# Kernel tuning notes

Measured on AMD Instinct MI355X. Metric: run time of the kernel, lower is better.

## Reference

```python
import jax, jax.numpy as jnp
import numpy as np

WINDOW = 3
SEQ_LEN = 41
FEATURE = 128
FILTER_NUM = 128
PAD = WINDOW // 2


def setup_inputs() -> dict:
    key = jax.random.key(0)
    k1, k2 = jax.random.split(key)
    B = 4096
    inputs = jax.random.normal(k1, (B, SEQ_LEN, FEATURE), dtype=jnp.float32)
    # per-position Linear weights: 41 independent [window*feature -> filter_num] layers
    fan_in = WINDOW * FEATURE
    W = jax.random.normal(k2, (SEQ_LEN, fan_in, FILTER_NUM), dtype=jnp.float32) / np.sqrt(fan_in)
    b = jnp.zeros((SEQ_LEN, FILTER_NUM), dtype=jnp.float32)
    return {"inputs": inputs, "W": W, "b": b}


def reference(inputs, W, b):
    # inputs: [B, S, F]; pad sequence dim by PAD zeros on each side
    xpad = jnp.pad(inputs, ((0, 0), (PAD, PAD), (0, 0)))  # [B, S+2*PAD, F]
    # gather windows: idx[s, w] = s + w -> [B, S, WINDOW, F]
    idx = jnp.arange(SEQ_LEN)[:, None] + jnp.arange(WINDOW)[None, :]
    xw = xpad[:, idx, :]
    B = inputs.shape[0]
    xw = xw.reshape(B, SEQ_LEN, WINDOW * FEATURE)  # [B, S, W*F]
    # per-position linear (locally-connected): one batched GEMM over positions
    out = jnp.einsum('bsd,sdf->bsf', xw, W) + b[None, :, :]
    # ReLU; Dropout(0.5) is identity in eval mode
    return jax.nn.relu(out)
```

## Files before the change

kernel.cpp:

```cpp
#include <hip/hip_runtime.h>
#include <hip/hip_bf16.h>

#define SEQ 41
#define FEAT 128
#define KDIM 384
#define BM 64
#define BK 64
#define LDA (BK + 8)
#define LDB (BK + 8)

typedef float floatx4 __attribute__((ext_vector_type(4)));
typedef __bf16 bf16x8 __attribute__((ext_vector_type(8)));
typedef unsigned short ushortx8 __attribute__((ext_vector_type(8)));

__device__ __forceinline__ unsigned short f2bf(float f) {
    unsigned int u = __builtin_bit_cast(unsigned int, f);
    unsigned int r = (u + 0x7fffu + ((u >> 16) & 1u)) >> 16;
    return (unsigned short)r;
}

__global__ __launch_bounds__(256) void wt_kernel(const float* __restrict__ W,
                                                 unsigned short* __restrict__ Wt) {
    int t = blockIdx.x * 256 + threadIdx.x;
    int n  = t & (FEAT - 1);
    int r  = t >> 7;
    int k0 = (r % (KDIM / 8)) * 8;
    int s  = r / (KDIM / 8);
    const float* Ws = W + (size_t)s * KDIM * FEAT;
    ushortx8 v;
#pragma unroll
    for (int j = 0; j < 8; j++) v[j] = f2bf(Ws[(size_t)(k0 + j) * FEAT + n]);
    *reinterpret_cast<ushortx8*>(Wt + ((size_t)(s * FEAT + n)) * KDIM + k0) = v;
}

template <int USE_WT>
__global__ __launch_bounds__(256) void gemm_kernel(const float* __restrict__ X,
                                                   const void* __restrict__ Wsrc,
                                                   const float* __restrict__ bias,
                                                   float* __restrict__ out) {
    __shared__ unsigned short Alds[BM][LDA];
    __shared__ unsigned short Blds[FEAT][LDB];

    const int tid = threadIdx.x;
    const int s   = blockIdx.y;
    const int m0  = blockIdx.x * BM;

    const int lane = tid & 63;
    const int wv   = tid >> 6;
    const int colq = lane & 15;
    const int quad = lane >> 4;
    const int arow = 16 * wv + colq;

    floatx4 acc[8];
#pragma unroll
    for (int nt = 0; nt < 8; nt++) acc[nt] = (floatx4){0.f, 0.f, 0.f, 0.f};

    const int a_row = tid & 63;
    const int a_seg = tid >> 6;
    const float* xrow = X + (size_t)(m0 + a_row) * (SEQ * FEAT);

    for (int kk = 0; kk < KDIM; kk += BK) {
        {
            int kbase = kk + a_seg * 16;
            int toff  = (s - 1) * FEAT + kbase;
            ushortx8 lo, hi;
#pragma unroll
            for (int j = 0; j < 4; j++) {
                int o = toff + j * 4;
                floatx4 v = (floatx4){0.f, 0.f, 0.f, 0.f};
                if (o >= 0 && o < SEQ * FEAT)
                    v = *reinterpret_cast<const floatx4*>(xrow + o);
#pragma unroll
                for (int e = 0; e < 4; e++) {
                    unsigned short b = f2bf(v[e]);
                    if (j < 2) lo[j * 4 + e] = b; else hi[(j - 2) * 4 + e] = b;
                }
            }
            *reinterpret_cast<ushortx8*>(&Alds[a_row][a_seg * 16])     = lo;
            *reinterpret_cast<ushortx8*>(&Alds[a_row][a_seg * 16 + 8]) = hi;
        }
        if (USE_WT) {
            const unsigned short* Wt = (const unsigned short*)Wsrc;
#pragma unroll
            for (int i = 0; i < 4; i++) {
                int chunk = i * 256 + tid;
                int n  = chunk >> 3;
                int c8 = (chunk & 7) << 3;
                ushortx8 v = *reinterpret_cast<const ushortx8*>(
                    Wt + ((size_t)(s * FEAT + n)) * KDIM + kk + c8);
                *reinterpret_cast<ushortx8*>(&Blds[n][c8]) = v;
            }
        } else {
            const float* Wf = (const float*)Wsrc;
#pragma unroll
            for (int i = 0; i < 8; i++) {
                int q  = i * 256 + tid;
                int n4 = (q & 31) * 4;
                int c  = q >> 5;
                floatx4 v = *reinterpret_cast<const floatx4*>(
                    Wf + ((size_t)(s * KDIM) + kk + c) * FEAT + n4);
#pragma unroll
                for (int j = 0; j < 4; j++) Blds[n4 + j][c] = f2bf(v[j]);
            }
        }
        __syncthreads();

#pragma unroll
        for (int ks = 0; ks < 2; ks++) {
            bf16x8 av = *reinterpret_cast<const bf16x8*>(&Alds[arow][ks * 32 + quad * 8]);
#pragma unroll
            for (int nt = 0; nt < 8; nt++) {
                bf16x8 bv = *reinterpret_cast<const bf16x8*>(
                    &Blds[nt * 16 + colq][ks * 32 + quad * 8]);
                acc[nt] = __builtin_amdgcn_mfma_f32_16x16x32_bf16(av, bv, acc[nt], 0, 0, 0);
            }
        }
        __syncthreads();
    }

    const int m_base = m0 + 16 * wv + quad * 4;
#pragma unroll
    for (int nt = 0; nt < 8; nt++) {
        int n = nt * 16 + colq;
        float bv = bias[s * FEAT + n];
#pragma unroll
        for (int r = 0; r < 4; r++) {
            float v = acc[nt][r] + bv;
            v = v > 0.f ? v : 0.f;
            out[((size_t)(m_base + r) * SEQ + s) * FEAT + n] = v;
        }
    }
}

extern "C" void kernel_launch(void* const* d_in, const int* in_sizes, int n_in,
                              void* d_out, int out_size, void* d_ws, size_t ws_size,
                              hipStream_t stream) {
    const float* X    = (const float*)d_in[0];
    const float* W    = (const float*)d_in[1];
    const float* bias = (const float*)d_in[2];
    float* out = (float*)d_out;

    const int B = in_sizes[0] / (SEQ * FEAT);
    dim3 grid(B / BM, SEQ);

    const size_t wt_bytes = (size_t)SEQ * FEAT * KDIM * sizeof(unsigned short);
    if (ws_size >= wt_bytes) {
        unsigned short* Wt = (unsigned short*)d_ws;
        wt_kernel<<<(SEQ * FEAT * (KDIM / 8) + 255) / 256, 256, 0, stream>>>(W, Wt);
        gemm_kernel<1><<<grid, 256, 0, stream>>>(X, (const void*)Wt, bias, out);
    } else {
        gemm_kernel<0><<<grid, 256, 0, stream>>>(X, (const void*)W, bias, out);
    }
}
```

Baseline: 210.2 us.

## Replace LDS-tiled GEMM with register-direct 32x32 MFMA and software prefetch

Drops shared-memory staging and barriers. Each wave now loads its A and B fragments directly from global memory into registers and feeds 32x32x16 bf16 MFMAs, with a one-step register prefetch of the next k-slice. The grid is reordered so the position index varies fastest, letting blocks that share input rows run close together, and each block covers 128 rows. In exchange, each wave reads B straight from global or L2 with no reuse through LDS, and the A loads are narrower per-lane accesses.

After: 256.9 us. +22.2%, slower.

```diff
diff --git a/kernel.cpp b/kernel.cpp
--- a/kernel.cpp
+++ b/kernel.cpp
@@ -4,12 +4,11 @@
 #define SEQ 41
 #define FEAT 128
 #define KDIM 384
-#define BM 64
-#define BK 64
-#define LDA (BK + 8)
-#define LDB (BK + 8)
+#define ROWLEN (SEQ * FEAT)
+#define KSTEPS (KDIM / 16)
 
 typedef float floatx4 __attribute__((ext_vector_type(4)));
+typedef float floatx16 __attribute__((ext_vector_type(16)));
 typedef __bf16 bf16x8 __attribute__((ext_vector_type(8)));
 typedef unsigned short ushortx8 __attribute__((ext_vector_type(8)));
 
@@ -17,6 +16,13 @@
     unsigned int u = __builtin_bit_cast(unsigned int, f);
     unsigned int r = (u + 0x7fffu + ((u >> 16) & 1u)) >> 16;
     return (unsigned short)r;
+}
+
+__device__ __forceinline__ bf16x8 cvt8(floatx4 lo, floatx4 hi) {
+    ushortx8 u;
+#pragma unroll
+    for (int j = 0; j < 4; j++) { u[j] = f2bf(lo[j]); u[4 + j] = f2bf(hi[j]); }
+    return __builtin_bit_cast(bf16x8, u);
 }
 
 __global__ __launch_bounds__(256) void wt_kernel(const float* __restrict__ W,
@@ -38,98 +44,88 @@
                                                    const void* __restrict__ Wsrc,
                                                    const float* __restrict__ bias,
                                                    float* __restrict__ out) {
-    __shared__ unsigned short Alds[BM][LDA];
-    __shared__ unsigned short Blds[FEAT][LDB];
-
-    const int tid = threadIdx.x;
-    const int s   = blockIdx.y;
-    const int m0  = blockIdx.x * BM;
-
+    const int tid  = threadIdx.x;
     const int lane = tid & 63;
     const int wv   = tid >> 6;
-    const int colq = lane & 15;
-    const int quad = lane >> 4;
-    const int arow = 16 * wv + colq;
+    const int s    = blockIdx.x;
+    const int mblk = blockIdx.y;
+    const int nl   = lane & 31;
+    const int kh   = lane >> 5;
 
-    floatx4 acc[8];
+    const int row = mblk * 128 + wv * 32 + nl;
+    const float* xrow = X + (size_t)row * ROWLEN;
+    const int obase = (s - 1) * FEAT + kh * 8;
+
+    const unsigned short* Wt = (const unsigned short*)Wsrc;
+    const float* Wf = (const float*)Wsrc;
+
+    floatx16 acc[4];
 #pragma unroll
-    for (int nt = 0; nt < 8; nt++) acc[nt] = (floatx4){0.f, 0.f, 0.f, 0.f};
+    for (int nt = 0; nt < 4; nt++) acc[nt] = (floatx16)(0.f);
 
-    const int a_row = tid & 63;
-    const int a_seg = tid >> 6;
-    const float* xrow = X + (size_t)(m0 + a_row) * (SEQ * FEAT);
+    floatx4 a_lo, a_hi;
+    ushortx8 bq[4];
 
-    for (int kk = 0; kk < KDIM; kk += BK) {
-        {
-            int kbase = kk + a_seg * 16;
-            int toff  = (s - 1) * FEAT + kbase;
-            ushortx8 lo, hi;
-#pragma unroll
-            for (int j = 0; j < 4; j++) {
-                int o = toff + j * 4;
-                floatx4 v = (floatx4){0.f, 0.f, 0.f, 0.f};
-                if (o >= 0 && o < SEQ * FEAT)
-                    v = *reinterpret_cast<const floatx4*>(xrow + o);
-#pragma unroll
-                for (int e = 0; e < 4; e++) {
-                    unsigned short b = f2bf(v[e]);
-                    if (j < 2) lo[j * 4 + e] = b; else hi[(j - 2) * 4 + e] = b;
-                }
-            }
-            *reinterpret_cast<ushortx8*>(&Alds[a_row][a_seg * 16])     = lo;
-            *reinterpret_cast<ushortx8*>(&Alds[a_row][a_seg * 16 + 8]) = hi;
-        }
-        if (USE_WT) {
-            const unsigned short* Wt = (const unsigned short*)Wsrc;
-#pragma unroll
-            for (int i = 0; i < 4; i++) {
-                int chunk = i * 256 + tid;
-                int n  = chunk >> 3;
-                int c8 = (chunk & 7) << 3;
-                ushortx8 v = *reinterpret_cast<const ushortx8*>(
-                    Wt + ((size_t)(s * FEAT + n)) * KDIM + kk + c8);
-                *reinterpret_cast<ushortx8*>(&Blds[n][c8]) = v;
-            }
-        } else {
-            const float* Wf = (const float*)Wsrc;
-#pragma unroll
-            for (int i = 0; i < 8; i++) {
-                int q  = i * 256 + tid;
-                int n4 = (q & 31) * 4;
-                int c  = q >> 5;
-                floatx4 v = *reinterpret_cast<const floatx4*>(
-                    Wf + ((size_t)(s * KDIM) + kk + c) * FEAT + n4);
-#pragma unroll
-                for (int j = 0; j < 4; j++) Blds[n4 + j][c] = f2bf(v[j]);
-            }
-        }
-        __syncthreads();
-
-#pragma unroll
-        for (int ks = 0; ks < 2; ks++) {
-            bf16x8 av = *reinterpret_cast<const bf16x8*>(&Alds[arow][ks * 32 + quad * 8]);
-#pragma unroll
-            for (int nt = 0; nt < 8; nt++) {
-                bf16x8 bv = *reinterpret_cast<const bf16x8*>(
-                    &Blds[nt * 16 + colq][ks * 32 + quad * 8]);
-                acc[nt] = __builtin_amdgcn_mfma_f32_16x16x32_bf16(av, bv, acc[nt], 0, 0, 0);
-            }
-        }
-        __syncthreads();
+#define LOAD_A(ks)                                                        \
+    {                                                                     \
+        int o = obase + (ks) * 16;                                        \
+        a_lo = (floatx4)(0.f); a_hi = (floatx4)(0.f);                     \
+        if (o >= 0 && o < ROWLEN) {                                       \
+            a_lo = *reinterpret_cast<const floatx4*>(xrow + o);           \
+            a_hi = *reinterpret_cast<const floatx4*>(xrow + o + 4);       \
+        }                                                                 \
+    }
+#define LOAD_B(ks)                                                              \
+    if (USE_WT) {                                                               \
+        _Pragma("unroll")                                                       \
+        for (int nt = 0; nt < 4; nt++)                                          \
+            bq[nt] = *reinterpret_cast<const ushortx8*>(                        \
+                Wt + ((size_t)(s * FEAT + nt * 32 + nl)) * KDIM + (ks) * 16 + kh * 8); \
+    } else {                                                                    \
+        _Pragma("unroll")                                                       \
+        for (int nt = 0; nt < 4; nt++) {                                        \
+            _Pragma("unroll")                                                   \
+            for (int j = 0; j < 8; j++)                                         \
+                bq[nt][j] = f2bf(Wf[((size_t)s * KDIM + (ks) * 16 + kh * 8 + j) * FEAT \
+                                    + nt * 32 + nl]);                           \
+        }                                                                       \
     }
 
-    const int m_base = m0 + 16 * wv + quad * 4;
+    LOAD_A(0);
+    LOAD_B(0);
+
+#pragma unroll 4
+    for (int ks = 0; ks < KSTEPS; ks++) {
+        bf16x8 av = cvt8(a_lo, a_hi);
+        bf16x8 bv0 = __builtin_bit_cast(bf16x8, bq[0]);
+        bf16x8 bv1 = __builtin_bit_cast(bf16x8, bq[1]);
+        bf16x8 bv2 = __builtin_bit_cast(bf16x8, bq[2]);
+        bf16x8 bv3 = __builtin_bit_cast(bf16x8, bq[3]);
+        if (ks + 1 < KSTEPS) {
+            LOAD_A(ks + 1);
+            LOAD_B(ks + 1);
+        }
+        acc[0] = __builtin_amdgcn_mfma_f32_32x32x16_bf16(av, bv0, acc[0], 0, 0, 0);
+        acc[1] = __builtin_amdgcn_mfma_f32_32x32x16_bf16(av, bv1, acc[1], 0, 0, 0);
+        acc[2] = __builtin_amdgcn_mfma_f32_32x32x16_bf16(av, bv2, acc[2], 0, 0, 0);
+        acc[3] = __builtin_amdgcn_mfma_f32_32x32x16_bf16(av, bv3, acc[3], 0, 0, 0);
+    }
+
+    const int mbase = mblk * 128 + wv * 32 + 4 * kh;
 #pragma unroll
-    for (int nt = 0; nt < 8; nt++) {
-        int n = nt * 16 + colq;
+    for (int nt = 0; nt < 4; nt++) {
+        int n = nt * 32 + nl;
         float bv = bias[s * FEAT + n];
 #pragma unroll
-        for (int r = 0; r < 4; r++) {
+        for (int r = 0; r < 16; r++) {
+            int m = mbase + (r & 3) + 8 * (r >> 2);
             float v = acc[nt][r] + bv;
             v = v > 0.f ? v : 0.f;
-            out[((size_t)(m_base + r) * SEQ + s) * FEAT + n] = v;
+            out[((size_t)m * SEQ + s) * FEAT + n] = v;
         }
     }
+#undef LOAD_A
+#undef LOAD_B
 }
 
 extern "C" void kernel_launch(void* const* d_in, const int* in_sizes, int n_in,
@@ -140,8 +136,8 @@
     const float* bias = (const float*)d_in[2];
     float* out = (float*)d_out;
 
-    const int B = in_sizes[0] / (SEQ * FEAT);
-    dim3 grid(B / BM, SEQ);
+    const int B = in_sizes[0] / ROWLEN;
+    dim3 grid(SEQ, B / 128);
 
     const size_t wt_bytes = (size_t)SEQ * FEAT * KDIM * sizeof(unsigned short);
     if (ws_size >= wt_bytes) {
```

## Double-buffer GEMM with fragment-ordered LDS, direct-to-LDS weight loads, and edge K-skip

Applied to the files above, without the earlier changes.

Rewrites the locally-connected GEMM to use a 128-row tile with a 2x2 wave layout, each wave computing a 4x4 grid of MFMA tiles. Weights are pre-permuted into MFMA fragment order so they can be copied global-to-LDS with direct DMA loads, and A tiles are written in fragment order. A register/LDS double buffer overlaps the next slab's loads with the current MFMAs, and K slabs that are entirely zero padding are skipped at the first and last sequence positions. The trade-off is more registers and LDS per block (launch bounds set to 2 blocks per CU) and halved grid size.

Result: faster. 184.2 us (-12.4%).

```diff
diff --git a/kernel.cpp b/kernel.cpp
--- a/kernel.cpp
+++ b/kernel.cpp
@@ -1,133 +1,170 @@
 #include <hip/hip_runtime.h>
-#include <hip/hip_bf16.h>
 
 #define SEQ 41
 #define FEAT 128
 #define KDIM 384
-#define BM 64
-#define BK 64
-#define LDA (BK + 8)
-#define LDB (BK + 8)
+#define ROWLEN (SEQ * FEAT)
+#define BM 128
 
 typedef float floatx4 __attribute__((ext_vector_type(4)));
 typedef __bf16 bf16x8 __attribute__((ext_vector_type(8)));
+typedef unsigned short ushortx4 __attribute__((ext_vector_type(4)));
 typedef unsigned short ushortx8 __attribute__((ext_vector_type(8)));
 
 __device__ __forceinline__ unsigned short f2bf(float f) {
     unsigned int u = __builtin_bit_cast(unsigned int, f);
-    unsigned int r = (u + 0x7fffu + ((u >> 16) & 1u)) >> 16;
-    return (unsigned short)r;
+    return (unsigned short)((u + 0x7fffu + ((u >> 16) & 1u)) >> 16);
 }
 
-__global__ __launch_bounds__(256) void wt_kernel(const float* __restrict__ W,
-                                                 unsigned short* __restrict__ Wt) {
+#define DMA16(g, l)                                                          \
+    __builtin_amdgcn_global_load_lds(                                        \
+        (const __attribute__((address_space(1))) void*)(g),                  \
+        (__attribute__((address_space(3))) void*)(l), 16, 0, 0)
+
+__global__ __launch_bounds__(256) void wt2_kernel(const float* __restrict__ W,
+                                                  unsigned short* __restrict__ Wt2) {
     int t = blockIdx.x * 256 + threadIdx.x;
-    int n  = t & (FEAT - 1);
-    int r  = t >> 7;
-    int k0 = (r % (KDIM / 8)) * 8;
-    int s  = r / (KDIM / 8);
+    int s = t / 6144, g = t % 6144;
+    int lane = g & 63, nt = (g >> 6) & 7, ks = (g >> 9) & 1, slab = g >> 10;
+    int n  = nt * 16 + (lane & 15);
+    int k0 = slab * 64 + ks * 32 + (lane >> 4) * 8;
     const float* Ws = W + (size_t)s * KDIM * FEAT;
     ushortx8 v;
 #pragma unroll
     for (int j = 0; j < 8; j++) v[j] = f2bf(Ws[(size_t)(k0 + j) * FEAT + n]);
-    *reinterpret_cast<ushortx8*>(Wt + ((size_t)(s * FEAT + n)) * KDIM + k0) = v;
+    *reinterpret_cast<ushortx8*>(Wt2 + (size_t)t * 8) = v;
 }
 
 template <int USE_WT>
-__global__ __launch_bounds__(256) void gemm_kernel(const float* __restrict__ X,
-                                                   const void* __restrict__ Wsrc,
-                                                   const float* __restrict__ bias,
-                                                   float* __restrict__ out) {
-    __shared__ unsigned short Alds[BM][LDA];
-    __shared__ unsigned short Blds[FEAT][LDB];
+__global__ __launch_bounds__(256, 2) void gemm_kernel(const float* __restrict__ X,
+                                                      const void* __restrict__ Wsrc,
+                                                      const float* __restrict__ bias,
+                                                      float* __restrict__ out) {
+    __shared__ unsigned short Afrag[2][2][8][512];
+    __shared__ unsigned short Bfrag[2][2][8][512];
 
-    const int tid = threadIdx.x;
-    const int s   = blockIdx.y;
-    const int m0  = blockIdx.x * BM;
-
+    const int tid  = threadIdx.x;
     const int lane = tid & 63;
     const int wv   = tid >> 6;
-    const int colq = lane & 15;
-    const int quad = lane >> 4;
-    const int arow = 16 * wv + colq;
+    const int s    = blockIdx.y;
+    const int m0   = blockIdx.x * BM;
 
-    floatx4 acc[8];
+    const int klo = (s == 0) ? 2 : 0;
+    const int khi = (s == SEQ - 1) ? 4 : 6;
+    const int nk  = khi - klo;
+    const int obase = (s - 1) * FEAT;
+
+    const int colq = lane & 15, quad = lane >> 4;
+    const int wr = wv >> 1, wc = wv & 1;
+
+    const int ar = tid >> 3;
+    const int ag = tid & 7;
+    const int aq = ag >> 1, ahalf = ag & 1;
+
+    const unsigned short* Wt2 = (const unsigned short*)Wsrc;
+    const float* Wf = (const float*)Wsrc;
+
+    floatx4 acc[4][4];
 #pragma unroll
-    for (int nt = 0; nt < 8; nt++) acc[nt] = (floatx4){0.f, 0.f, 0.f, 0.f};
+    for (int i = 0; i < 4; i++)
+#pragma unroll
+        for (int j = 0; j < 4; j++) acc[i][j] = (floatx4){0.f, 0.f, 0.f, 0.f};
 
-    const int a_row = tid & 63;
-    const int a_seg = tid >> 6;
-    const float* xrow = X + (size_t)(m0 + a_row) * (SEQ * FEAT);
+    floatx4 a0[4], a1[4];
 
-    for (int kk = 0; kk < KDIM; kk += BK) {
-        {
-            int kbase = kk + a_seg * 16;
-            int toff  = (s - 1) * FEAT + kbase;
-            ushortx8 lo, hi;
+    auto stageA_load = [&](int kki) {
+#pragma unroll
+        for (int p = 0; p < 4; p++) {
+            const float* base = X + (size_t)(m0 + p * 32 + ar) * ROWLEN
+                                  + obase + kki * 64 + ag * 4;
+            a0[p] = *reinterpret_cast<const floatx4*>(base);
+            a1[p] = *reinterpret_cast<const floatx4*>(base + 32);
+        }
+    };
+    auto stageA_write = [&](int buf) {
+#pragma unroll
+        for (int p = 0; p < 4; p++) {
+            int r  = p * 32 + ar;
+            int mt = r >> 4;
+            int sl = ((r & 15) + 16 * aq) * 8 + ahalf * 4;
+            ushortx4 w0, w1;
+#pragma unroll
+            for (int e = 0; e < 4; e++) { w0[e] = f2bf(a0[p][e]); w1[e] = f2bf(a1[p][e]); }
+            *reinterpret_cast<ushortx4*>(&Afrag[buf][0][mt][sl]) = w0;
+            *reinterpret_cast<ushortx4*>(&Afrag[buf][1][mt][sl]) = w1;
+        }
+    };
+    auto stageB = [&](int buf, int kki) {
+        if (USE_WT) {
+            const unsigned short* src = Wt2 + (size_t)(s * 6 + kki) * 8192;
 #pragma unroll
             for (int j = 0; j < 4; j++) {
-                int o = toff + j * 4;
-                floatx4 v = (floatx4){0.f, 0.f, 0.f, 0.f};
-                if (o >= 0 && o < SEQ * FEAT)
-                    v = *reinterpret_cast<const floatx4*>(xrow + o);
-#pragma unroll
-                for (int e = 0; e < 4; e++) {
-                    unsigned short b = f2bf(v[e]);
-                    if (j < 2) lo[j * 4 + e] = b; else hi[(j - 2) * 4 + e] = b;
-                }
-            }
-            *reinterpret_cast<ushortx8*>(&Alds[a_row][a_seg * 16])     = lo;
-            *reinterpret_cast<ushortx8*>(&Alds[a_row][a_seg * 16 + 8]) = hi;
-        }
-        if (USE_WT) {
-            const unsigned short* Wt = (const unsigned short*)Wsrc;
-#pragma unroll
-            for (int i = 0; i < 4; i++) {
-                int chunk = i * 256 + tid;
-                int n  = chunk >> 3;
-                int c8 = (chunk & 7) << 3;
-                ushortx8 v = *reinterpret_cast<const ushortx8*>(
-                    Wt + ((size_t)(s * FEAT + n)) * KDIM + kk + c8);
-                *reinterpret_cast<ushortx8*>(&Blds[n][c8]) = v;
+                int fid = wv * 4 + j;
+                const unsigned short* g = src + fid * 512 + lane * 8;
+                DMA16(g, &Bfrag[buf][fid >> 3][fid & 7][0]);
             }
         } else {
-            const float* Wf = (const float*)Wsrc;
 #pragma unroll
-            for (int i = 0; i < 8; i++) {
-                int q  = i * 256 + tid;
-                int n4 = (q & 31) * 4;
-                int c  = q >> 5;
-                floatx4 v = *reinterpret_cast<const floatx4*>(
-                    Wf + ((size_t)(s * KDIM) + kk + c) * FEAT + n4);
+            for (int p = 0; p < 4; p++) {
+                int g2 = p * 256 + tid;
+                int ln = g2 & 63, nt = (g2 >> 6) & 7, ks = (g2 >> 9) & 1;
+                int n = nt * 16 + (ln & 15);
+                int k = kki * 64 + ks * 32 + (ln >> 4) * 8;
+                ushortx8 v;
 #pragma unroll
-                for (int j = 0; j < 4; j++) Blds[n4 + j][c] = f2bf(v[j]);
+                for (int j = 0; j < 8; j++)
+                    v[j] = f2bf(Wf[((size_t)s * KDIM + k + j) * FEAT + n]);
+                *reinterpret_cast<ushortx8*>(&Bfrag[buf][ks][nt][ln * 8]) = v;
             }
         }
+    };
+    auto compute = [&](int buf) {
+#pragma unroll
+        for (int ks = 0; ks < 2; ks++) {
+            bf16x8 af[4], bf[4];
+#pragma unroll
+            for (int i = 0; i < 4; i++)
+                af[i] = *reinterpret_cast<const bf16x8*>(&Afrag[buf][ks][wr * 4 + i][lane * 8]);
+#pragma unroll
+            for (int i = 0; i < 4; i++)
+                bf[i] = *reinterpret_cast<const bf16x8*>(&Bfrag[buf][ks][wc * 4 + i][lane * 8]);
+#pragma unroll
+            for (int mi = 0; mi < 4; mi++)
+#pragma unroll
+                for (int ni = 0; ni < 4; ni++)
+                    acc[mi][ni] = __builtin_amdgcn_mfma_f32_16x16x32_bf16(
+                        af[mi], bf[ni], acc[mi][ni], 0, 0, 0);
+        }
+    };
+
+    stageA_load(klo);
+    stageB(0, klo);
+    stageA_write(0);
+
+    for (int i = 0; i < nk; i++) {
         __syncthreads();
+        int cur = i & 1, nxt = cur ^ 1;
+        if (i + 1 < nk) {
+            stageA_load(klo + i + 1);
+            stageB(nxt, klo + i + 1);
+        }
+        compute(cur);
+        if (i + 1 < nk) stageA_write(nxt);
+    }
 
 #pragma unroll
-        for (int ks = 0; ks < 2; ks++) {
-            bf16x8 av = *reinterpret_cast<const bf16x8*>(&Alds[arow][ks * 32 + quad * 8]);
+    for (int mi = 0; mi < 4; mi++) {
+        int m = m0 + (wr * 4 + mi) * 16 + quad * 4;
 #pragma unroll
-            for (int nt = 0; nt < 8; nt++) {
-                bf16x8 bv = *reinterpret_cast<const bf16x8*>(
-                    &Blds[nt * 16 + colq][ks * 32 + quad * 8]);
-                acc[nt] = __builtin_amdgcn_mfma_f32_16x16x32_bf16(av, bv, acc[nt], 0, 0, 0);
+        for (int ni = 0; ni < 4; ni++) {
+            int n = (wc * 4 + ni) * 16 + colq;
+            float bv = bias[s * FEAT + n];
+#pragma unroll
+            for (int r = 0; r < 4; r++) {
+                float v = acc[mi][ni][r] + bv;
+                v = v > 0.f ? v : 0.f;
+                out[((size_t)(m + r) * SEQ + s) * FEAT + n] = v;
             }
-        }
-        __syncthreads();
-    }
-
-    const int m_base = m0 + 16 * wv + quad * 4;
-#pragma unroll
-    for (int nt = 0; nt < 8; nt++) {
-        int n = nt * 16 + colq;
-        float bv = bias[s * FEAT + n];
-#pragma unroll
-        for (int r = 0; r < 4; r++) {
-            float v = acc[nt][r] + bv;
-            v = v > 0.f ? v : 0.f;
-            out[((size_t)(m_base + r) * SEQ + s) * FEAT + n] = v;
         }
     }
 }
@@ -140,14 +177,14 @@
     const float* bias = (const float*)d_in[2];
     float* out = (float*)d_out;
 
-    const int B = in_sizes[0] / (SEQ * FEAT);
+    const int B = in_sizes[0] / ROWLEN;
     dim3 grid(B / BM, SEQ);
 
-    const size_t wt_bytes = (size_t)SEQ * FEAT * KDIM * sizeof(unsigned short);
+    const size_t wt_bytes = (size_t)SEQ * 6 * 8192 * sizeof(unsigned short);
     if (ws_size >= wt_bytes) {
-        unsigned short* Wt = (unsigned short*)d_ws;
-        wt_kernel<<<(SEQ * FEAT * (KDIM / 8) + 255) / 256, 256, 0, stream>>>(W, Wt);
-        gemm_kernel<1><<<grid, 256, 0, stream>>>(X, (const void*)Wt, bias, out);
+        unsigned short* Wt2 = (unsigned short*)d_ws;
+        wt2_kernel<<<(SEQ * 6144) / 256, 256, 0, stream>>>(W, Wt2);
+        gemm_kernel<1><<<grid, 256, 0, stream>>>(X, (const void*)Wt2, bias, out);
     } else {
         gemm_kernel<0><<<grid, 256, 0, stream>>>(X, (const void*)W, bias, out);
     }
```
